# Kernel optimization log

Measured on AMD Instinct MI355X. Metric: run time of the kernel, lower is better.

The kernel has to match this reference:

```python
import jax, jax.numpy as jnp
import numpy as np

N_NODES = 50000
N_EDGES = 800000
N_FEAT = 128
N_GRAPHS = 512
OUT_DIM = 128


def gcn_conv(x, W, b, src, dst, ew, n):
    """PyG GCNConv: h = x @ W; add self-loops (weight 1); symmetric norm
    D^-1/2 A D^-1/2 with edge weights; scatter-add messages src->dst; + bias."""
    h = x @ W  # [n, out]
    loop = jnp.arange(n)
    s = jnp.concatenate([src, loop])
    d = jnp.concatenate([dst, loop])
    w = jnp.concatenate([ew, jnp.ones((n,), x.dtype)])
    deg = jax.ops.segment_sum(w, d, num_segments=n)
    dinv = jnp.where(deg > 0, jax.lax.rsqrt(deg), 0.0)
    norm = dinv[s] * w * dinv[d]  # [E+n]
    out = jax.ops.segment_sum(h[s] * norm[:, None], d, num_segments=n)
    return out + b


def setup_inputs() -> dict:
    key = jax.random.key(0)
    ks = jax.random.split(key, 12)
    F = N_FEAT
    x = jax.random.normal(ks[0], (N_NODES, F), jnp.float32)
    edge_index = jax.random.randint(ks[1], (2, N_EDGES), 0, N_NODES, jnp.int64)
    edge_attr = jax.random.uniform(ks[2], (N_EDGES,), jnp.float32)
    # deterministic sorted graph assignment -> no empty graphs (avoids -inf in max pool)
    batch = (jnp.arange(N_NODES, dtype=jnp.int64) * N_GRAPHS) // N_NODES
    def lin(k, fi, fo):
        s = 1.0 / np.sqrt(fi)
        return jax.random.uniform(k, (fi, fo), jnp.float32, -s, s)
    return {
        "x": x, "edge_attr": edge_attr,
        "W1": lin(ks[3], F, F), "b1": jnp.zeros((F,), jnp.float32),
        "W2": lin(ks[4], F, 2 * F), "b2": jnp.zeros((2 * F,), jnp.float32),
        "W3": lin(ks[5], 2 * F, 4 * F), "b3": jnp.zeros((4 * F,), jnp.float32),
        "Wf1": lin(ks[6], 4 * F, 1024), "bf1": jnp.zeros((1024,), jnp.float32),
        "Wf2": lin(ks[7], 1024, OUT_DIM), "bf2": jnp.zeros((OUT_DIM,), jnp.float32),
        "edge_index": edge_index, "batch": batch,
    }


def reference(x, edge_attr, W1, b1, W2, b2, W3, b3, Wf1, bf1, Wf2, bf2,
              edge_index, batch):
    n = x.shape[0]
    src, dst = edge_index[0], edge_index[1]
    h = jax.nn.relu(gcn_conv(x, W1, b1, src, dst, edge_attr, n))
    h = jax.nn.relu(gcn_conv(h, W2, b2, src, dst, edge_attr, n))
    h = jax.nn.relu(gcn_conv(h, W3, b3, src, dst, edge_attr, n))
    # global max pool over nodes per graph
    g = jax.ops.segment_max(h, batch, num_segments=N_GRAPHS)  # [G, 4F]
    g = jax.nn.relu(g @ Wf1 + bf1)
    # dropout is identity in eval mode
    out = g @ Wf2 + bf2
    return out
```

## Files before the change

### kernel.cpp

```cpp
#include <hip/hip_runtime.h>

#define NNODES 50000
#define NPAD   50048
#define NEDGES 800000
#define NGRAPH 512
#define DCAP 64

typedef short bf16x8 __attribute__((ext_vector_type(8)));
typedef unsigned short u16x8 __attribute__((ext_vector_type(8)));
typedef float f32x4 __attribute__((ext_vector_type(4)));
typedef unsigned long long u64;

#define GLOAD16(g, l)                                                                 \
    __builtin_amdgcn_global_load_lds((const __attribute__((address_space(1))) unsigned*)(g), \
                                     (__attribute__((address_space(3))) unsigned*)(l), 16, 0, 0)

static __device__ __forceinline__ float b2f(unsigned short u) {
    return __uint_as_float(((unsigned)u) << 16);
}
static __device__ __forceinline__ unsigned short f2b(float f) {
    unsigned u = __float_as_uint(f);
    unsigned r = (u + 0x7fffu + ((u >> 16) & 1u)) >> 16;
    return (unsigned short)r;
}

static __device__ __forceinline__ void accum8(float (&acc)[8], float c, uint4 v) {
    unsigned w[4] = {v.x, v.y, v.z, v.w};
    #pragma unroll
    for (int i = 0; i < 4; ++i) {
        acc[2 * i]     += c * __uint_as_float(w[i] << 16);
        acc[2 * i + 1] += c * __uint_as_float(w[i] & 0xffff0000u);
    }
}

#define EBLK 782
__global__ __launch_bounds__(256) void k_pre(const float* __restrict__ W1, const float* __restrict__ W2,
                                             const float* __restrict__ W3, const float* __restrict__ Wf1,
                                             const float* __restrict__ Wf2,
                                             unsigned short* __restrict__ T1, unsigned short* __restrict__ T2,
                                             unsigned short* __restrict__ T3, unsigned short* __restrict__ Tf1,
                                             unsigned short* __restrict__ Tf2,
                                             const int4* __restrict__ ei_s, const int4* __restrict__ ei_d,
                                             const float4* __restrict__ ew4,
                                             u64* deg_cnt, unsigned* __restrict__ edges,
                                             const float* __restrict__ x, unsigned short* __restrict__ x16) {
    const int b = blockIdx.x;
    if (b < EBLK) {
        int t = b * 256 + threadIdx.x;
        if (t >= NEDGES / 4) return;
        int4 ss = ei_s[t];
        int4 dd = ei_d[t];
        float4 ww = ew4[t];
        int s[4] = {ss.x, ss.y, ss.z, ss.w};
        int d[4] = {dd.x, dd.y, dd.z, dd.w};
        float w[4] = {ww.x, ww.y, ww.z, ww.w};
        int slot[4];
        #pragma unroll
        for (int u = 0; u < 4; ++u) {
            unsigned fixed = __float2uint_rn(w[u] * 16777216.0f);
            u64 old = atomicAdd(&deg_cnt[d[u]], ((u64)1 << 32) | fixed);
            slot[u] = (int)(old >> 32);
            if (slot[u] > DCAP - 1) slot[u] = DCAP - 1;
        }
        #pragma unroll
        for (int u = 0; u < 4; ++u)
            edges[((unsigned)d[u] << 6) | slot[u]] = ((unsigned)f2b(w[u]) << 16) | (unsigned)s[u];
        return;
    }
    if (b < EBLK + 204) {
        const int bb = b - EBLK;
        const float* W; unsigned short* T; int K, N, t0;
        if (bb < 4)        { W = W1;  T = T1;  K = 128;  N = 128;  t0 = 0;   }
        else if (bb < 12)  { W = W2;  T = T2;  K = 128;  N = 256;  t0 = 4;   }
        else if (bb < 44)  { W = W3;  T = T3;  K = 256;  N = 512;  t0 = 12;  }
        else if (bb < 172) { W = Wf1; T = Tf1; K = 512;  N = 1024; t0 = 44;  }
        else               { W = Wf2; T = Tf2; K = 1024; N = 128;  t0 = 172; }
        const int tile = bb - t0;
        const int ntn = N >> 6;
        const int k0 = (tile / ntn) * 64, n0 = (tile % ntn) * 64;
        __shared__ float sm[64][65];
        const int t = threadIdx.x;
        const int rr = t >> 6, cc = t & 63;
        #pragma unroll
        for (int r = 0; r < 16; ++r) {
            int kl = r * 4 + rr;
            sm[kl][cc] = W[(size_t)(k0 + kl) * N + n0 + cc];
        }
        __syncthreads();
        #pragma unroll
        for (int r = 0; r < 16; ++r) {
            int nl = r * 4 + rr;
            T[(size_t)(n0 + nl) * K + k0 + cc] = f2b(sm[cc][nl]);
        }
        return;
    }
    int idx = (b - EBLK - 204) * 256 + threadIdx.x;
    if (idx < NNODES * 16) {
        float4 v0 = ((const float4*)x)[idx * 2];
        float4 v1 = ((const float4*)x)[idx * 2 + 1];
        uint4 o;
        o.x = (unsigned)f2b(v0.x) | ((unsigned)f2b(v0.y) << 16);
        o.y = (unsigned)f2b(v0.z) | ((unsigned)f2b(v0.w) << 16);
        o.z = (unsigned)f2b(v1.x) | ((unsigned)f2b(v1.y) << 16);
        o.w = (unsigned)f2b(v1.z) | ((unsigned)f2b(v1.w) << 16);
        ((uint4*)x16)[idx] = o;
    }
}

__global__ void k_prep(const u64* __restrict__ deg_cnt, float* __restrict__ dinv, int* __restrict__ gp) {
    int i = blockIdx.x * 256 + threadIdx.x;
    if (i < NNODES)
        dinv[i] = rsqrtf((float)(unsigned)(deg_cnt[i] & 0xffffffffull) * 5.9604645e-8f + 1.0f);
    if (i < NGRAPH * 512) gp[i] = 0;
}

template <int F, int SLICES, bool DSRC>
__global__ __launch_bounds__(256) void k_aggregate(const unsigned short* __restrict__ X,
                                                   const u64* __restrict__ deg_cnt,
                                                   const unsigned* __restrict__ edges,
                                                   const float* __restrict__ dinv,
                                                   unsigned short* __restrict__ Z) {
    constexpr int FS = F / SLICES;
    constexpr int LPR = FS / 8;
    constexpr int GRP = 64 / LPR;
    constexpr int STEP = GRP * 2;
    const int bid = blockIdx.x;
    const int slice = (SLICES == 1) ? 0 : (bid & (SLICES - 1));
    const int chunk = (SLICES == 1) ? bid : (bid / SLICES);
    const int wave = threadIdx.x >> 6, lane = threadIdx.x & 63;
    const int node = chunk * 4 + wave;
    if (node >= NNODES) return;
    const int sub = lane & (LPR - 1);
    const int grp = lane / LPR;
    const int fo = slice * FS + sub * 8;
    const unsigned short* Xf = X + fo;
    const float di = dinv[node];
    const int cnt = (int)(deg_cnt[node] >> 32);
    const unsigned* erow = edges + ((unsigned)node << 6);

    const uint4 selfv = *(const uint4*)(Xf + (size_t)node * F);

    float acc[8] = {};

    const int e0 = grp;
    const int nb = (cnt + STEP - 1) / STEP;

    unsigned pa0 = 0, pb0 = 0, pa1 = 0, pb1 = 0;
    uint4 va0 = {}, vb0 = {};
    float da0 = 1.f, db0 = 1.f;
    if (nb > 0) {
        int ea = e0, eb = e0 + GRP;
        pa0 = (ea < cnt) ? erow[ea] : 0u;
        pb0 = (eb < cnt) ? erow[eb] : 0u;
        va0 = *(const uint4*)(Xf + (size_t)(pa0 & 0xffffu) * F);
        vb0 = *(const uint4*)(Xf + (size_t)(pb0 & 0xffffu) * F);
        if constexpr (DSRC) { da0 = dinv[pa0 & 0xffffu]; db0 = dinv[pb0 & 0xffffu]; }
        if (nb > 1) {
            int ea1 = e0 + STEP, eb1 = ea1 + GRP;
            pa1 = (ea1 < cnt) ? erow[ea1] : 0u;
            pb1 = (eb1 < cnt) ? erow[eb1] : 0u;
        }
    }
    for (int p = 0; p < nb; ++p) {
        uint4 va1 = {}, vb1 = {};
        float da1 = 1.f, db1 = 1.f;
        unsigned pa2 = 0, pb2 = 0;
        if (p + 1 < nb) {
            va1 = *(const uint4*)(Xf + (size_t)(pa1 & 0xffffu) * F);
            vb1 = *(const uint4*)(Xf + (size_t)(pb1 & 0xffffu) * F);
            if constexpr (DSRC) { da1 = dinv[pa1 & 0xffffu]; db1 = dinv[pb1 & 0xffffu]; }
            if (p + 2 < nb) {
                int ea = e0 + (p + 2) * STEP, eb = ea + GRP;
                pa2 = (ea < cnt) ? erow[ea] : 0u;
                pb2 = (eb < cnt) ? erow[eb] : 0u;
            }
        }
        float ca = b2f((unsigned short)(pa0 >> 16));
        float cb = b2f((unsigned short)(pb0 >> 16));
        if constexpr (DSRC) { ca *= da0; cb *= db0; }
        accum8(acc, ca, va0);
        accum8(acc, cb, vb0);
        pa0 = pa1; pb0 = pb1; va0 = va1; vb0 = vb1;
        da0 = da1; db0 = db1;
        pa1 = pa2; pb1 = pb2;
    }

    #pragma unroll
    for (int j = 0; j < 8; ++j) {
        if constexpr (GRP == 4) acc[j] += __shfl_xor(acc[j], 16, 64);
        acc[j] += __shfl_xor(acc[j], 32, 64);
    }

    if (grp == 0) {
        const float sc = DSRC ? di : 1.0f;
        unsigned w[4] = {selfv.x, selfv.y, selfv.z, selfv.w};
        unsigned o[4];
        #pragma unroll
        for (int i = 0; i < 4; ++i) {
            float s0 = __uint_as_float(w[i] << 16);
            float s1 = __uint_as_float(w[i] & 0xffff0000u);
            unsigned short c0 = f2b(di * (acc[2 * i] + sc * s0));
            unsigned short c1 = f2b(di * (acc[2 * i + 1] + sc * s1));
            o[i] = (unsigned)c0 | ((unsigned)c1 << 16);
        }
        uint4 ov; ov.x = o[0]; ov.y = o[1]; ov.z = o[2]; ov.w = o[3];
        *(uint4*)(Z + (size_t)node * F + fo) = ov;
    }
}

template <int CMODE>
__global__ __launch_bounds__(256) void k_gemm128(const unsigned short* __restrict__ A,
                                                 const unsigned short* __restrict__ WT,
                                                 const float* __restrict__ bias,
                                                 unsigned short* __restrict__ C,
                                                 const int* __restrict__ batch,
                                                 int* __restrict__ gp,
                                                 const float* __restrict__ rscale,
                                                 int M, int N, int K) {
    __shared__ unsigned short As[2][128 * 32];
    __shared__ unsigned short Bs[2][128 * 32];
    const int tid = threadIdx.x;

    const int nwg = gridDim.x * gridDim.y;
    const int f = blockIdx.y * gridDim.x + blockIdx.x;
    const int q = nwg >> 3, r = nwg & 7;
    const int xcd = f & 7, idx = f >> 3;
    const int w = (xcd < r) ? xcd * (q + 1) + idx : r * (q + 1) + (xcd - r) * q + idx;
    const int m0 = (w / gridDim.x) * 128;
    const int n0 = (w % gridDim.x) * 128;

    const int wave = tid >> 6, lane = tid & 63;
    const int wm = (wave >> 1) * 64, wn = (wave & 1) * 64;
    const int quad = lane >> 4, mrow = lane & 15;

    const int sr = tid >> 2;
    const int sc = (tid & 3) * 8;
    const unsigned short* Ag0 = A + (size_t)(m0 + sr) * K + sc;
    const unsigned short* Ag1 = A + (size_t)(m0 + 64 + sr) * K + sc;
    const unsigned short* Bg0 = WT + (size_t)(n0 + sr) * K + sc;
    const unsigned short* Bg1 = WT + (size_t)(n0 + 64 + sr) * K + sc;
    const int so0 = sr * 32 + sc, so1 = (64 + sr) * 32 + sc;

    f32x4 acc[4][4] = {};
    const int nsteps = K >> 5;

    GLOAD16(Ag0, &As[0][so0]);
    GLOAD16(Ag1, &As[0][so1]);
    GLOAD16(Bg0, &Bs[0][so0]);
    GLOAD16(Bg1, &Bs[0][so1]);
    __syncthreads();

    for (int step = 0; step < nsteps; ++step) {
        const int cur = step & 1;
        if (step + 1 < nsteps) {
            const int k1 = (step + 1) << 5;
            GLOAD16(Ag0 + k1, &As[cur ^ 1][so0]);
            GLOAD16(Ag1 + k1, &As[cur ^ 1][so1]);
            GLOAD16(Bg0 + k1, &Bs[cur ^ 1][so0]);
            GLOAD16(Bg1 + k1, &Bs[cur ^ 1][so1]);
        }
        bf16x8 af[4], bf[4];
        #pragma unroll
        for (int mt = 0; mt < 4; ++mt)
            af[mt] = *(const bf16x8*)&As[cur][(wm + mt * 16 + mrow) * 32 + quad * 8];
        #pragma unroll
        for (int nt = 0; nt < 4; ++nt)
            bf[nt] = *(const bf16x8*)&Bs[cur][(wn + nt * 16 + mrow) * 32 + quad * 8];
        #pragma unroll
        for (int mt = 0; mt < 4; ++mt)
            #pragma unroll
            for (int nt = 0; nt < 4; ++nt)
                acc[mt][nt] = __builtin_amdgcn_mfma_f32_16x16x32_bf16(af[mt], bf[nt], acc[mt][nt], 0, 0, 0);
        __syncthreads();
    }

    float bn[4];
    #pragma unroll
    for (int nt = 0; nt < 4; ++nt) bn[nt] = bias[n0 + wn + nt * 16 + mrow];

    if constexpr (CMODE == 0) {
        #pragma unroll
        for (int mt = 0; mt < 4; ++mt) {
            #pragma unroll
            for (int r4 = 0; r4 < 4; ++r4) {
                int row = m0 + wm + mt * 16 + quad * 4 + r4;
                if (row < M) {
                    float rs = rscale ? rscale[row] : 1.0f;
                    #pragma unroll
                    for (int nt = 0; nt < 4; ++nt) {
                        float v = fmaxf(acc[mt][nt][r4] + bn[nt], 0.f) * rs;
                        C[(size_t)row * N + n0 + wn + nt * 16 + mrow] = f2b(v);
                    }
                }
            }
        }
    } else {
        const int wr0 = m0 + wm;
        int g0i = wr0 < M ? wr0 : M - 1;
        const int g0 = batch[g0i];
        int lastr = wr0 + 63; if (lastr >= M) lastr = M - 1;
        const int gl = batch[lastr];
        bool rok[16]; int gid[16];
        #pragma unroll
        for (int mt = 0; mt < 4; ++mt)
            #pragma unroll
            for (int r4 = 0; r4 < 4; ++r4) {
                int row = wr0 + mt * 16 + quad * 4 + r4;
                rok[mt * 4 + r4] = row < M;
                gid[mt * 4 + r4] = (row < M) ? batch[row] : -1;
            }
        #pragma unroll
        for (int nt = 0; nt < 4; ++nt) {
            float v0 = 0.f, v1 = 0.f;
            #pragma unroll
            for (int mt = 0; mt < 4; ++mt)
                #pragma unroll
                for (int r4 = 0; r4 < 4; ++r4)
                    if (rok[mt * 4 + r4]) {
                        float v = fmaxf(acc[mt][nt][r4] + bn[nt], 0.f);
                        if (gid[mt * 4 + r4] == g0) v0 = fmaxf(v0, v);
                        else v1 = fmaxf(v1, v);
                    }
            v0 = fmaxf(v0, __shfl_xor(v0, 16, 64));
            v0 = fmaxf(v0, __shfl_xor(v0, 32, 64));
            v1 = fmaxf(v1, __shfl_xor(v1, 16, 64));
            v1 = fmaxf(v1, __shfl_xor(v1, 32, 64));
            if (quad == 0) {
                int c = n0 + wn + nt * 16 + mrow;
                atomicMax(&gp[(size_t)g0 * N + c], __float_as_int(v0));
                if (gl != g0) atomicMax(&gp[(size_t)gl * N + c], __float_as_int(v1));
            }
        }
    }
}

template <int CMODE, int AFP>
__global__ __launch_bounds__(256) void k_gemm_mfma(const void* __restrict__ Av,
                                                   const unsigned short* __restrict__ WT,
                                                   const float* __restrict__ bias,
                                                   void* __restrict__ Cv,
                                                   int M, int N, int K) {
    constexpr int LDK = 40;
    __shared__ unsigned short As[64 * LDK];
    __shared__ unsigned short Bs[128 * LDK];
    const int tid = threadIdx.x;
    const int m0 = blockIdx.y * 64, n0 = blockIdx.x * 128;
    const int wave = tid >> 6, lane = tid & 63;
    const int wm = (wave >> 1) * 32;
    const int wn = (wave & 1) * 64;
    const int quad = lane >> 4, mrow = lane & 15;

    const int ar = tid >> 2;
    const int ak = (tid & 3) * 8;
    const bool arow_ok = (m0 + ar) < M;
    const size_t aoff = (size_t)(m0 + ar) * K + ak;
    const unsigned short* Bg0 = WT + (size_t)(n0 + ar) * K + ak;
    const unsigned short* Bg1 = WT + (size_t)(n0 + ar + 64) * K + ak;

    f32x4 acc[2][4] = {};

    for (int k0 = 0; k0 < K; k0 += 32) {
        u16x8 av = {};
        if (arow_ok) {
            if constexpr (AFP) {
                const float* Af = (const float*)Av + aoff + k0;
                float4 f0 = *(const float4*)Af;
                float4 f1 = *(const float4*)(Af + 4);
                av[0] = (short)f2b(f0.x); av[1] = (short)f2b(f0.y);
                av[2] = (short)f2b(f0.z); av[3] = (short)f2b(f0.w);
                av[4] = (short)f2b(f1.x); av[5] = (short)f2b(f1.y);
                av[6] = (short)f2b(f1.z); av[7] = (short)f2b(f1.w);
            } else {
                av = *(const u16x8*)((const unsigned short*)Av + aoff + k0);
            }
        }
        u16x8 bv0 = *(const u16x8*)(Bg0 + k0);
        u16x8 bv1 = *(const u16x8*)(Bg1 + k0);
        *(u16x8*)&As[ar * LDK + ak] = av;
        *(u16x8*)&Bs[ar * LDK + ak] = bv0;
        *(u16x8*)&Bs[(ar + 64) * LDK + ak] = bv1;
        __syncthreads();
        bf16x8 af[2], bf[4];
        #pragma unroll
        for (int mt = 0; mt < 2; ++mt)
            af[mt] = *(const bf16x8*)&As[(wm + mt * 16 + mrow) * LDK + quad * 8];
        #pragma unroll
        for (int nt = 0; nt < 4; ++nt)
            bf[nt] = *(const bf16x8*)&Bs[(wn + nt * 16 + mrow) * LDK + quad * 8];
        #pragma unroll
        for (int mt = 0; mt < 2; ++mt)
            #pragma unroll
            for (int nt = 0; nt < 4; ++nt)
                acc[mt][nt] = __builtin_amdgcn_mfma_f32_16x16x32_bf16(af[mt], bf[nt], acc[mt][nt], 0, 0, 0);
        __syncthreads();
    }

    float bn[4];
    #pragma unroll
    for (int nt = 0; nt < 4; ++nt) bn[nt] = bias[n0 + wn + nt * 16 + mrow];

    if constexpr (CMODE == 0) {
        unsigned short* C = (unsigned short*)Cv;
        #pragma unroll
        for (int mt = 0; mt < 2; ++mt) {
            #pragma unroll
            for (int r = 0; r < 4; ++r) {
                int row = m0 + wm + mt * 16 + quad * 4 + r;
                if (row < M) {
                    #pragma unroll
                    for (int nt = 0; nt < 4; ++nt) {
                        float v = fmaxf(acc[mt][nt][r] + bn[nt], 0.f);
                        C[(size_t)row * N + n0 + wn + nt * 16 + mrow] = f2b(v);
                    }
                }
            }
        }
    } else {
        float* C = (float*)Cv;
        #pragma unroll
        for (int mt = 0; mt < 2; ++mt) {
            #pragma unroll
            for (int r = 0; r < 4; ++r) {
                int row = m0 + wm + mt * 16 + quad * 4 + r;
                if (row < M) {
                    #pragma unroll
                    for (int nt = 0; nt < 4; ++nt)
                        C[(size_t)row * N + n0 + wn + nt * 16 + mrow] = acc[mt][nt][r] + bn[nt];
                }
            }
        }
    }
}

extern "C" void kernel_launch(void* const* d_in, const int* in_sizes, int n_in,
                              void* d_out, int out_size, void* d_ws, size_t ws_size,
                              hipStream_t stream) {
    const float* x   = (const float*)d_in[0];
    const float* ew  = (const float*)d_in[1];
    const float* W1  = (const float*)d_in[2];
    const float* b1  = (const float*)d_in[3];
    const float* W2  = (const float*)d_in[4];
    const float* b2  = (const float*)d_in[5];
    const float* W3  = (const float*)d_in[6];
    const float* b3  = (const float*)d_in[7];
    const float* Wf1 = (const float*)d_in[8];
    const float* bf1 = (const float*)d_in[9];
    const float* Wf2 = (const float*)d_in[10];
    const float* bf2 = (const float*)d_in[11];
    const int* ei    = (const int*)d_in[12];
    const int* batch = (const int*)d_in[13];
    float* out = (float*)d_out;
    (void)in_sizes; (void)n_in; (void)out_size; (void)ws_size;

    char* p = (char*)d_ws;
    auto alloc = [&](size_t bytes) -> char* {
        char* r = p;
        p += (bytes + 255) & ~(size_t)255;
        return r;
    };
    u64*   deg_cnt = (u64*)alloc((size_t)NNODES * 8);
    float* dinv   = (float*)alloc((size_t)NNODES * 4);
    unsigned* edges = (unsigned*)alloc((size_t)NNODES * DCAP * 4);
    int*   gp     = (int*)  alloc((size_t)NGRAPH * 512 * 4);
    unsigned short* f1   = (unsigned short*)alloc((size_t)NGRAPH * 1024 * 2);
    unsigned short* wt1  = (unsigned short*)alloc((size_t)128 * 128 * 2);
    unsigned short* wt2  = (unsigned short*)alloc((size_t)256 * 128 * 2);
    unsigned short* wt3  = (unsigned short*)alloc((size_t)512 * 256 * 2);
    unsigned short* wtf1 = (unsigned short*)alloc((size_t)1024 * 512 * 2);
    unsigned short* wtf2 = (unsigned short*)alloc((size_t)128 * 1024 * 2);
    unsigned short* bufA = (unsigned short*)alloc((size_t)NPAD * 256 * 2);
    unsigned short* bufB = (unsigned short*)alloc((size_t)NPAD * 256 * 2);
    unsigned short* x16  = bufB;

    const int MB128 = (NNODES + 127) / 128;
    const int AGG = (NNODES + 3) / 4;
    const int CVB = (NNODES * 16 + 255) / 256;

    hipMemsetAsync(deg_cnt, 0, (size_t)NNODES * 8, stream);
    k_pre<<<EBLK + 204 + CVB, 256, 0, stream>>>(W1, W2, W3, Wf1, Wf2,
                                                wt1, wt2, wt3, wtf1, wtf2,
                                                (const int4*)ei, (const int4*)(ei + NEDGES),
                                                (const float4*)ew, deg_cnt, edges, x, x16);
    k_prep<<<1024, 256, 0, stream>>>(deg_cnt, dinv, gp);

    k_aggregate<128, 1, true><<<AGG, 256, 0, stream>>>(x16, deg_cnt, edges, dinv, bufA);
    k_gemm128<0><<<dim3(1, MB128), 256, 0, stream>>>(bufA, wt1, b1, bufB, nullptr, nullptr, dinv, NNODES, 128, 128);
    k_aggregate<128, 1, false><<<AGG, 256, 0, stream>>>(bufB, deg_cnt, edges, dinv, bufA);
    k_gemm128<0><<<dim3(2, MB128), 256, 0, stream>>>(bufA, wt2, b2, bufB, nullptr, nullptr, dinv, NNODES, 256, 128);
    k_aggregate<256, 2, false><<<AGG * 2, 256, 0, stream>>>(bufB, deg_cnt, edges, dinv, bufA);
    k_gemm128<2><<<dim3(4, MB128), 256, 0, stream>>>(bufA, wt3, b3, nullptr, batch, gp, nullptr, NNODES, 512, 256);

    k_gemm_mfma<0, 1><<<dim3(8, NGRAPH / 64), 256, 0, stream>>>(gp, wtf1, bf1, f1, NGRAPH, 1024, 512);
    k_gemm_mfma<1, 0><<<dim3(1, NGRAPH / 64), 256, 0, stream>>>(f1, wtf2, bf2, out, NGRAPH, 128, 1024);
}
```

Measured before the change: 364.9 us.

## Fuse layer-1 GEMM into prep kernel and move bias/ReLU into aggregate epilogue

The x→bf16 conversion pass is replaced by an MFMA GEMM computing x@W1 inside the preprocessing kernel, so layer 1 multiplies before aggregating instead of after. The separate layer-1 GEMM launch goes away: bias, ReLU and the next layer's dinv pre-scale are applied in the first aggregate's epilogue, and layer 2 then aggregates directly. This removes one kernel launch and one full node-feature round trip through memory. The cost is a larger shared-memory footprint for every k_pre block, and the GEMM blocks now run concurrently with the atomic edge-binning blocks.

```diff
diff --git a/kernel.cpp b/kernel.cpp
--- a/kernel.cpp
+++ b/kernel.cpp
@@ -34,19 +34,23 @@
 }
 
 #define EBLK 782
+#define TBLK 200
+#define GBLK 782
 __global__ __launch_bounds__(256) void k_pre(const float* __restrict__ W1, const float* __restrict__ W2,
                                              const float* __restrict__ W3, const float* __restrict__ Wf1,
                                              const float* __restrict__ Wf2,
-                                             unsigned short* __restrict__ T1, unsigned short* __restrict__ T2,
+                                             unsigned short* __restrict__ T2,
                                              unsigned short* __restrict__ T3, unsigned short* __restrict__ Tf1,
                                              unsigned short* __restrict__ Tf2,
                                              const int4* __restrict__ ei_s, const int4* __restrict__ ei_d,
                                              const float4* __restrict__ ew4,
                                              u64* deg_cnt, unsigned* __restrict__ edges,
-                                             const float* __restrict__ x, unsigned short* __restrict__ x16) {
+                                             const float* __restrict__ x, unsigned short* __restrict__ P1) {
+    __shared__ __align__(16) char smem[38912];
     const int b = blockIdx.x;
+    const int tid = threadIdx.x;
     if (b < EBLK) {
-        int t = b * 256 + threadIdx.x;
+        int t = b * 256 + tid;
         if (t >= NEDGES / 4) return;
         int4 ss = ei_s[t];
         int4 dd = ei_d[t];
@@ -67,20 +71,18 @@
             edges[((unsigned)d[u] << 6) | slot[u]] = ((unsigned)f2b(w[u]) << 16) | (unsigned)s[u];
         return;
     }
-    if (b < EBLK + 204) {
+    if (b < EBLK + TBLK) {
         const int bb = b - EBLK;
         const float* W; unsigned short* T; int K, N, t0;
-        if (bb < 4)        { W = W1;  T = T1;  K = 128;  N = 128;  t0 = 0;   }
-        else if (bb < 12)  { W = W2;  T = T2;  K = 128;  N = 256;  t0 = 4;   }
-        else if (bb < 44)  { W = W3;  T = T3;  K = 256;  N = 512;  t0 = 12;  }
-        else if (bb < 172) { W = Wf1; T = Tf1; K = 512;  N = 1024; t0 = 44;  }
-        else               { W = Wf2; T = Tf2; K = 1024; N = 128;  t0 = 172; }
+        if (bb < 8)        { W = W2;  T = T2;  K = 128;  N = 256;  t0 = 0;   }
+        else if (bb < 40)  { W = W3;  T = T3;  K = 256;  N = 512;  t0 = 8;   }
+        else if (bb < 168) { W = Wf1; T = Tf1; K = 512;  N = 1024; t0 = 40;  }
+        else               { W = Wf2; T = Tf2; K = 1024; N = 128;  t0 = 168; }
         const int tile = bb - t0;
         const int ntn = N >> 6;
         const int k0 = (tile / ntn) * 64, n0 = (tile % ntn) * 64;
-        __shared__ float sm[64][65];
-        const int t = threadIdx.x;
-        const int rr = t >> 6, cc = t & 63;
+        float (*sm)[65] = (float(*)[65])smem;
+        const int rr = tid >> 6, cc = tid & 63;
         #pragma unroll
         for (int r = 0; r < 16; ++r) {
             int kl = r * 4 + rr;
@@ -94,17 +96,65 @@
         }
         return;
     }
-    int idx = (b - EBLK - 204) * 256 + threadIdx.x;
-    if (idx < NNODES * 16) {
-        float4 v0 = ((const float4*)x)[idx * 2];
-        float4 v1 = ((const float4*)x)[idx * 2 + 1];
-        uint4 o;
-        o.x = (unsigned)f2b(v0.x) | ((unsigned)f2b(v0.y) << 16);
-        o.y = (unsigned)f2b(v0.z) | ((unsigned)f2b(v0.w) << 16);
-        o.z = (unsigned)f2b(v1.x) | ((unsigned)f2b(v1.y) << 16);
-        o.w = (unsigned)f2b(v1.z) | ((unsigned)f2b(v1.w) << 16);
-        ((uint4*)x16)[idx] = o;
-    }
+    const int gb = b - EBLK - TBLK;
+    const int m0 = gb * 64;
+    unsigned short* BsT = (unsigned short*)smem;
+    unsigned short* As  = (unsigned short*)(smem + 33792);
+    const float4* W1v = (const float4*)W1;
+    #pragma unroll
+    for (int i = 0; i < 16; ++i) {
+        int idx = i * 256 + tid;
+        int k = idx >> 5, q = idx & 31;
+        float4 v = W1v[idx];
+        int n = q * 4;
+        BsT[(n + 0) * 132 + k] = f2b(v.x);
+        BsT[(n + 1) * 132 + k] = f2b(v.y);
+        BsT[(n + 2) * 132 + k] = f2b(v.z);
+        BsT[(n + 3) * 132 + k] = f2b(v.w);
+    }
+    const int wave = tid >> 6, lane = tid & 63;
+    const int wm = (wave >> 1) * 32, wn = (wave & 1) * 64;
+    const int quad = lane >> 4, mrow = lane & 15;
+    const int ar = tid >> 2, ak = (tid & 3) * 8;
+    const bool arow_ok = (m0 + ar) < NNODES;
+    f32x4 acc[2][4] = {};
+    __syncthreads();
+    for (int k0 = 0; k0 < 128; k0 += 32) {
+        u16x8 av = {};
+        if (arow_ok) {
+            const float* Af = x + (size_t)(m0 + ar) * 128 + k0 + ak;
+            float4 f0 = *(const float4*)Af;
+            float4 f1 = *(const float4*)(Af + 4);
+            av[0] = (short)f2b(f0.x); av[1] = (short)f2b(f0.y);
+            av[2] = (short)f2b(f0.z); av[3] = (short)f2b(f0.w);
+            av[4] = (short)f2b(f1.x); av[5] = (short)f2b(f1.y);
+            av[6] = (short)f2b(f1.z); av[7] = (short)f2b(f1.w);
+        }
+        *(u16x8*)&As[ar * 40 + ak] = av;
+        __syncthreads();
+        bf16x8 af[2], bf[4];
+        #pragma unroll
+        for (int mt = 0; mt < 2; ++mt)
+            af[mt] = *(const bf16x8*)&As[(wm + mt * 16 + mrow) * 40 + quad * 8];
+        #pragma unroll
+        for (int nt = 0; nt < 4; ++nt)
+            bf[nt] = *(const bf16x8*)&BsT[(wn + nt * 16 + mrow) * 132 + k0 + quad * 8];
+        #pragma unroll
+        for (int mt = 0; mt < 2; ++mt)
+            #pragma unroll
+            for (int nt = 0; nt < 4; ++nt)
+                acc[mt][nt] = __builtin_amdgcn_mfma_f32_16x16x32_bf16(af[mt], bf[nt], acc[mt][nt], 0, 0, 0);
+        __syncthreads();
+    }
+    #pragma unroll
+    for (int mt = 0; mt < 2; ++mt)
+        #pragma unroll
+        for (int r = 0; r < 4; ++r) {
+            int row = m0 + wm + mt * 16 + quad * 4 + r;
+            #pragma unroll
+            for (int nt = 0; nt < 4; ++nt)
+                P1[(size_t)row * 128 + wn + nt * 16 + mrow] = f2b(acc[mt][nt][r]);
+        }
 }
 
 __global__ void k_prep(const u64* __restrict__ deg_cnt, float* __restrict__ dinv, int* __restrict__ gp) {
@@ -114,12 +164,13 @@
     if (i < NGRAPH * 512) gp[i] = 0;
 }
 
-template <int F, int SLICES, bool DSRC>
+template <int F, int SLICES, bool DSRC, bool EPI>
 __global__ __launch_bounds__(256) void k_aggregate(const unsigned short* __restrict__ X,
                                                    const u64* __restrict__ deg_cnt,
                                                    const unsigned* __restrict__ edges,
                                                    const float* __restrict__ dinv,
-                                                   unsigned short* __restrict__ Z) {
+                                                   unsigned short* __restrict__ Z,
+                                                   const float* __restrict__ bias) {
     constexpr int FS = F / SLICES;
     constexpr int LPR = FS / 8;
     constexpr int GRP = 64 / LPR;
@@ -192,6 +243,13 @@
     }
 
     if (grp == 0) {
+        float bv[8];
+        if constexpr (EPI) {
+            float4 q0 = *(const float4*)(bias + fo);
+            float4 q1 = *(const float4*)(bias + fo + 4);
+            bv[0] = q0.x; bv[1] = q0.y; bv[2] = q0.z; bv[3] = q0.w;
+            bv[4] = q1.x; bv[5] = q1.y; bv[6] = q1.z; bv[7] = q1.w;
+        }
         const float sc = DSRC ? di : 1.0f;
         unsigned w[4] = {selfv.x, selfv.y, selfv.z, selfv.w};
         unsigned o[4];
@@ -199,9 +257,13 @@
         for (int i = 0; i < 4; ++i) {
             float s0 = __uint_as_float(w[i] << 16);
             float s1 = __uint_as_float(w[i] & 0xffff0000u);
-            unsigned short c0 = f2b(di * (acc[2 * i] + sc * s0));
-            unsigned short c1 = f2b(di * (acc[2 * i + 1] + sc * s1));
-            o[i] = (unsigned)c0 | ((unsigned)c1 << 16);
+            float z0 = di * (acc[2 * i] + sc * s0);
+            float z1 = di * (acc[2 * i + 1] + sc * s1);
+            if constexpr (EPI) {
+                z0 = di * fmaxf(z0 + bv[2 * i], 0.f);
+                z1 = di * fmaxf(z1 + bv[2 * i + 1], 0.f);
+            }
+            o[i] = (unsigned)f2b(z0) | ((unsigned)f2b(z1) << 16);
         }
         uint4 ov; ov.x = o[0]; ov.y = o[1]; ov.z = o[2]; ov.w = o[3];
         *(uint4*)(Z + (size_t)node * F + fo) = ov;
@@ -463,32 +525,29 @@
     unsigned* edges = (unsigned*)alloc((size_t)NNODES * DCAP * 4);
     int*   gp     = (int*)  alloc((size_t)NGRAPH * 512 * 4);
     unsigned short* f1   = (unsigned short*)alloc((size_t)NGRAPH * 1024 * 2);
-    unsigned short* wt1  = (unsigned short*)alloc((size_t)128 * 128 * 2);
     unsigned short* wt2  = (unsigned short*)alloc((size_t)256 * 128 * 2);
     unsigned short* wt3  = (unsigned short*)alloc((size_t)512 * 256 * 2);
     unsigned short* wtf1 = (unsigned short*)alloc((size_t)1024 * 512 * 2);
     unsigned short* wtf2 = (unsigned short*)alloc((size_t)128 * 1024 * 2);
     unsigned short* bufA = (unsigned short*)alloc((size_t)NPAD * 256 * 2);
     unsigned short* bufB = (unsigned short*)alloc((size_t)NPAD * 256 * 2);
-    unsigned short* x16  = bufB;
+    unsigned short* P1   = bufB;
 
     const int MB128 = (NNODES + 127) / 128;
     const int AGG = (NNODES + 3) / 4;
-    const int CVB = (NNODES * 16 + 255) / 256;
 
     hipMemsetAsync(deg_cnt, 0, (size_t)NNODES * 8, stream);
-    k_pre<<<EBLK + 204 + CVB, 256, 0, stream>>>(W1, W2, W3, Wf1, Wf2,
-                                                wt1, wt2, wt3, wtf1, wtf2,
-                                                (const int4*)ei, (const int4*)(ei + NEDGES),
-                                                (const float4*)ew, deg_cnt, edges, x, x16);
+    k_pre<<<EBLK + TBLK + GBLK, 256, 0, stream>>>(W1, W2, W3, Wf1, Wf2,
+                                                  wt2, wt3, wtf1, wtf2,
+                                                  (const int4*)ei, (const int4*)(ei + NEDGES),
+                                                  (const float4*)ew, deg_cnt, edges, x, P1);
     k_prep<<<1024, 256, 0, stream>>>(deg_cnt, dinv, gp);
 
-    k_aggregate<128, 1, true><<<AGG, 256, 0, stream>>>(x16, deg_cnt, edges, dinv, bufA);
-    k_gemm128<0><<<dim3(1, MB128), 256, 0, stream>>>(bufA, wt1, b1, bufB, nullptr, nullptr, dinv, NNODES, 128, 128);
-    k_aggregate<128, 1, false><<<AGG, 256, 0, stream>>>(bufB, deg_cnt, edges, dinv, bufA);
-    k_gemm128<0><<<dim3(2, MB128), 256, 0, stream>>>(bufA, wt2, b2, bufB, nullptr, nullptr, dinv, NNODES, 256, 128);
-    k_aggregate<256, 2, false><<<AGG * 2, 256, 0, stream>>>(bufB, deg_cnt, edges, dinv, bufA);
-    k_gemm128<2><<<dim3(4, MB128), 256, 0, stream>>>(bufA, wt3, b3, nullptr, batch, gp, nullptr, NNODES, 512, 256);
+    k_aggregate<128, 1, true, true><<<AGG, 256, 0, stream>>>(P1, deg_cnt, edges, dinv, bufA, b1);
+    k_aggregate<128, 1, false, false><<<AGG, 256, 0, stream>>>(bufA, deg_cnt, edges, dinv, bufB, nullptr);
+    k_gemm128<0><<<dim3(2, MB128), 256, 0, stream>>>(bufB, wt2, b2, bufA, nullptr, nullptr, dinv, NNODES, 256, 128);
+    k_aggregate<256, 2, false, false><<<AGG * 2, 256, 0, stream>>>(bufA, deg_cnt, edges, dinv, bufB, nullptr);
+    k_gemm128<2><<<dim3(4, MB128), 256, 0, stream>>>(bufB, wt3, b3, nullptr, batch, gp, nullptr, NNODES, 512, 256);
 
     k_gemm_mfma<0, 1><<<dim3(8, NGRAPH / 64), 256, 0, stream>>>(gp, wtf1, bf1, f1, NGRAPH, 1024, 512);
     k_gemm_mfma<1, 0><<<dim3(1, NGRAPH / 64), 256, 0, stream>>>(f1, wtf2, bf2, out, NGRAPH, 128, 1024);
```

New measurement: 361.2 us. About the same (-1.0%).
